# Performance work log

Measured on AMD Instinct MI355X. Metric: run time of the kernel, lower is better.

## Reference

```python
import jax, jax.numpy as jnp
import numpy as np

L, B, D = 50, 1024, 512      # memory slots, batch, d_model
H, DK = 4, 512               # heads, per-head dim (d_k = d_model in this module)
HOP = 3


def setup_inputs() -> dict:
    key = jax.random.key(0)
    ks = jax.random.split(key, 16)
    s = lambda i, shape: jax.random.normal(ks[i], shape, jnp.float32) * 0.02
    return dict(
        momery=jax.random.normal(ks[0], (L, B, D), jnp.float32),
        hid=jax.random.normal(ks[1], (B, D), jnp.float32),
        text_polarity=jax.random.normal(ks[2], (B,), jnp.float32),
        attribute_polarity=jax.random.normal(ks[3], (B,), jnp.float32),
        w=jnp.array(0.5, jnp.float32),
        p_w1=s(4, (D, D)), p_b1=jnp.zeros((D,), jnp.float32),
        p_w2=s(5, (D, D)), p_b2=jnp.zeros((D,), jnp.float32),
        wq=s(6, (D, H * DK)), bq=jnp.zeros((H * DK,), jnp.float32),
        wk=s(7, (D, H * DK)), bk=jnp.zeros((H * DK,), jnp.float32),
        wv=s(8, (D, H * DK)), bv=jnp.zeros((H * DK,), jnp.float32),
        wo=s(9, (H * DK, D)), bo=jnp.zeros((D,), jnp.float32),
    )


def reference(momery, hid, text_polarity, attribute_polarity, w,
              p_w1, p_b1, p_w2, p_b2, wq, bq, wk, bk, wv, bv, wo, bo):
    # k, v depend only on hid (attinkv = hid every hop/slot) -> hoist out of hop loop
    k = (hid @ wk + bk).reshape(B, H, DK)   # [B,H,DK]
    v = (hid @ wv + bv).reshape(B, H, DK)   # [B,H,DK]
    inv_sqrt_dk = jnp.float32(1.0 / np.sqrt(DK))
    for _ in range(HOP):
        # projection MLP over all slots at once (replaces per-slot loop)
        mid = jax.nn.relu(momery @ p_w1 + p_b1) @ p_w2 + p_b2          # [L,B,D]
        q = (mid @ wq + bq).reshape(L, B, H, DK)                        # [L,B,H,DK]
        # single key per query (nk=1): scores [L,B,H,1], softmax -> ones
        scores = (jnp.einsum('lbhd,bhd->lbh', q, k) * inv_sqrt_dk)[..., None]
        att = jax.nn.softmax(scores, axis=-1)                           # [L,B,H,1]
        out = att * v                                                   # [L,B,H,DK]
        temp = out.reshape(L, B, H * DK) @ wo + bo                      # [L,B,D]
        momery = momery + w * temp
    return momery
```

## Files before the change

kernel.cpp:

```cpp
#include <hip/hip_runtime.h>

#define B_SZ 1024
#define D_SZ 512
#define LDSP 68

template <int K, int KCHUNK>
__device__ __forceinline__ void gemm_body(const float* __restrict__ A,
                                          const float* __restrict__ B,
                                          float* __restrict__ C, int N,
                                          int row0, int col0, int zk) {
    __shared__ float As[32 * LDSP];
    __shared__ float Bs[32 * LDSP];

    const int tid = threadIdx.x;
    const int k0  = zk * KCHUNK;
    constexpr int NT = KCHUNK / 32;

    const int aR = tid >> 3;
    const int aK = (tid & 7) << 2;
    const int bK = tid >> 4;
    const int bC = (tid & 15) << 2;

    const int ty = (tid >> 4) << 2;
    const int tx = (tid & 15) << 2;

    const float* pa0 = A + (size_t)(row0 + aR) * K + k0 + aK;
    const float* pa1 = pa0 + (size_t)32 * K;
    const float* pb0 = B + (size_t)(k0 + bK) * N + col0 + bC;
    const float* pb1 = pb0 + (size_t)16 * N;

    float4 a0 = *(const float4*)pa0;
    float4 a1 = *(const float4*)pa1;
    float4 b0 = *(const float4*)pb0;
    float4 b1 = *(const float4*)pb1;

    float acc[4][4] = {};

    for (int t = 0; t < NT; ++t) {
        __syncthreads();
        As[(aK + 0) * LDSP + aR] = a0.x;
        As[(aK + 1) * LDSP + aR] = a0.y;
        As[(aK + 2) * LDSP + aR] = a0.z;
        As[(aK + 3) * LDSP + aR] = a0.w;
        As[(aK + 0) * LDSP + aR + 32] = a1.x;
        As[(aK + 1) * LDSP + aR + 32] = a1.y;
        As[(aK + 2) * LDSP + aR + 32] = a1.z;
        As[(aK + 3) * LDSP + aR + 32] = a1.w;
        *(float4*)(Bs + bK * LDSP + bC) = b0;
        *(float4*)(Bs + (bK + 16) * LDSP + bC) = b1;
        if (t + 1 < NT) {
            pa0 += 32; pa1 += 32;
            pb0 += (size_t)32 * N; pb1 += (size_t)32 * N;
            a0 = *(const float4*)pa0;
            a1 = *(const float4*)pa1;
            b0 = *(const float4*)pb0;
            b1 = *(const float4*)pb1;
        }
        __syncthreads();
#pragma unroll
        for (int kk = 0; kk < 32; ++kk) {
            float4 av = *(const float4*)(As + kk * LDSP + ty);
            float4 bv = *(const float4*)(Bs + kk * LDSP + tx);
            float ar[4] = {av.x, av.y, av.z, av.w};
            float br[4] = {bv.x, bv.y, bv.z, bv.w};
#pragma unroll
            for (int i = 0; i < 4; ++i)
#pragma unroll
                for (int j = 0; j < 4; ++j) acc[i][j] += ar[i] * br[j];
        }
    }

    const int r0 = row0 + ty;
    const int c0 = col0 + tx;
#pragma unroll
    for (int i = 0; i < 4; ++i)
#pragma unroll
        for (int j = 0; j < 4; ++j)
            atomicAdd(&C[(size_t)(r0 + i) * N + c0 + j], acc[i][j]);
}

__global__ __launch_bounds__(256) void gemmA_bias(const float* __restrict__ wv,
                                                  const float* __restrict__ wo,
                                                  const float* __restrict__ bv,
                                                  const float* __restrict__ bo,
                                                  float* __restrict__ W,
                                                  float* __restrict__ b2) {
    if (blockIdx.z == 4) {
        int bid = blockIdx.y * 8 + blockIdx.x;
        int g = bid * 256 + threadIdx.x;
        int o = g & 511;
        int r = g >> 9;
        float s = 0.f;
        int j0 = r * 64;
#pragma unroll 8
        for (int j = j0; j < j0 + 64; ++j) s += bv[j] * wo[j * 512 + o];
        if (r == 0) s += bo[o];
        atomicAdd(&b2[o], s);
        return;
    }
    gemm_body<2048, 512>(wv, wo, W, 512, blockIdx.y * 64, blockIdx.x * 64,
                         blockIdx.z);
}

__global__ __launch_bounds__(256) void gemmB(const float* __restrict__ hid,
                                             const float* __restrict__ W,
                                             float* __restrict__ temp) {
    gemm_body<512, 256>(hid, W, temp, 512, blockIdx.y * 64, blockIdx.x * 64,
                        blockIdx.z);
}

__global__ __launch_bounds__(256) void bcast_add_kernel(const float* __restrict__ mem,
                                                        const float* __restrict__ temp,
                                                        const float* __restrict__ b2,
                                                        const float* __restrict__ wp,
                                                        float* __restrict__ out) {
    int idx = blockIdx.x * 256 + threadIdx.x;
    const float4 mv = ((const float4*)mem)[idx];
    int bd = idx & ((B_SZ * D_SZ / 4) - 1);
    const float4 tv = ((const float4*)temp)[bd];
    const float4 bb = ((const float4*)b2)[bd & 127];
    float s = 3.0f * wp[0];
    float4 o;
    o.x = mv.x + s * (tv.x + bb.x);
    o.y = mv.y + s * (tv.y + bb.y);
    o.z = mv.z + s * (tv.z + bb.z);
    o.w = mv.w + s * (tv.w + bb.w);
    ((float4*)out)[idx] = o;
}

extern "C" void kernel_launch(void* const* d_in, const int* in_sizes, int n_in,
                              void* d_out, int out_size, void* d_ws, size_t ws_size,
                              hipStream_t stream) {
    const float* momery = (const float*)d_in[0];
    const float* hid    = (const float*)d_in[1];
    const float* w      = (const float*)d_in[4];
    const float* wv     = (const float*)d_in[13];
    const float* bv     = (const float*)d_in[14];
    const float* wo     = (const float*)d_in[15];
    const float* bo     = (const float*)d_in[16];
    float* out = (float*)d_out;

    float* W    = (float*)d_ws;
    float* b2   = W + 512 * 512;
    float* temp = b2 + 512;
    size_t zbytes = (size_t)(512 * 512 + 512 + 1024 * 512) * sizeof(float);

    hipMemsetAsync(d_ws, 0, zbytes, stream);

    gemmA_bias<<<dim3(8, 8, 5), 256, 0, stream>>>(wv, wo, bv, bo, W, b2);

    gemmB<<<dim3(8, 16, 2), 256, 0, stream>>>(hid, W, temp);

    bcast_add_kernel<<<25600, 256, 0, stream>>>(momery, temp, b2, w, out);
}
```

Measured before the change: 288.6 us.

## Replace atomic split-K accumulation with partial buffers and drop workspace memset

The split-K GEMMs now write per-split partial results to separate workspace slices with plain float4 stores instead of atomicAdd. The second GEMM sums the four partial W slices as it loads them, and folds the bias partials into its z=0 output. The final broadcast kernel adds the two temp halves. This removes the memset launch and the atomic traffic, at the cost of more workspace and extra reads of the partial buffers.

```diff
diff --git a/kernel.cpp b/kernel.cpp
--- a/kernel.cpp
+++ b/kernel.cpp
@@ -4,29 +4,36 @@
 #define D_SZ 512
 #define LDSP 68
 
-template <int K, int KCHUNK>
-__device__ __forceinline__ void gemm_body(const float* __restrict__ A,
-                                          const float* __restrict__ B,
-                                          float* __restrict__ C, int N,
-                                          int row0, int col0, int zk) {
+__device__ __forceinline__ float4 f4add(float4 a, float4 b) {
+    return make_float4(a.x + b.x, a.y + b.y, a.z + b.z, a.w + b.w);
+}
+
+__global__ __launch_bounds__(256) void gemmA(const float* __restrict__ wv,
+                                             const float* __restrict__ wo,
+                                             const float* __restrict__ bv,
+                                             const float* __restrict__ bo,
+                                             float* __restrict__ Wp,
+                                             float* __restrict__ b2p) {
     __shared__ float As[32 * LDSP];
     __shared__ float Bs[32 * LDSP];
 
-    const int tid = threadIdx.x;
-    const int k0  = zk * KCHUNK;
-    constexpr int NT = KCHUNK / 32;
+    const int tid  = threadIdx.x;
+    const int col0 = blockIdx.x * 64;
+    const int row0 = blockIdx.y * 64;
+    const int z    = blockIdx.z;
+    const int k0   = z * 512;
+    constexpr int K = 2048, N = 512, NT = 16;
 
     const int aR = tid >> 3;
     const int aK = (tid & 7) << 2;
     const int bK = tid >> 4;
     const int bC = (tid & 15) << 2;
-
     const int ty = (tid >> 4) << 2;
     const int tx = (tid & 15) << 2;
 
-    const float* pa0 = A + (size_t)(row0 + aR) * K + k0 + aK;
+    const float* pa0 = wv + (size_t)(row0 + aR) * K + k0 + aK;
     const float* pa1 = pa0 + (size_t)32 * K;
-    const float* pb0 = B + (size_t)(k0 + bK) * N + col0 + bC;
+    const float* pb0 = wo + (size_t)(k0 + bK) * N + col0 + bC;
     const float* pb1 = pb0 + (size_t)16 * N;
 
     float4 a0 = *(const float4*)pa0;
@@ -60,9 +67,9 @@
 #pragma unroll
         for (int kk = 0; kk < 32; ++kk) {
             float4 av = *(const float4*)(As + kk * LDSP + ty);
-            float4 bv = *(const float4*)(Bs + kk * LDSP + tx);
+            float4 bv4 = *(const float4*)(Bs + kk * LDSP + tx);
             float ar[4] = {av.x, av.y, av.z, av.w};
-            float br[4] = {bv.x, bv.y, bv.z, bv.w};
+            float br[4] = {bv4.x, bv4.y, bv4.z, bv4.w};
 #pragma unroll
             for (int i = 0; i < 4; ++i)
 #pragma unroll
@@ -70,61 +77,139 @@
         }
     }
 
-    const int r0 = row0 + ty;
-    const int c0 = col0 + tx;
+    float* C = Wp + (size_t)z * 262144;
+    const int r0 = row0 + ty, c0 = col0 + tx;
 #pragma unroll
     for (int i = 0; i < 4; ++i)
-#pragma unroll
-        for (int j = 0; j < 4; ++j)
-            atomicAdd(&C[(size_t)(r0 + i) * N + c0 + j], acc[i][j]);
-}
-
-__global__ __launch_bounds__(256) void gemmA_bias(const float* __restrict__ wv,
-                                                  const float* __restrict__ wo,
-                                                  const float* __restrict__ bv,
-                                                  const float* __restrict__ bo,
-                                                  float* __restrict__ W,
-                                                  float* __restrict__ b2) {
-    if (blockIdx.z == 4) {
+        *(float4*)(C + (size_t)(r0 + i) * N + c0) =
+            make_float4(acc[i][0], acc[i][1], acc[i][2], acc[i][3]);
+
+    if (z == 0) {
         int bid = blockIdx.y * 8 + blockIdx.x;
-        int g = bid * 256 + threadIdx.x;
+        int g = bid * 256 + tid;
         int o = g & 511;
         int r = g >> 9;
-        float s = 0.f;
+        float s = (r == 0) ? bo[o] : 0.f;
         int j0 = r * 64;
 #pragma unroll 8
         for (int j = j0; j < j0 + 64; ++j) s += bv[j] * wo[j * 512 + o];
-        if (r == 0) s += bo[o];
-        atomicAdd(&b2[o], s);
-        return;
-    }
-    gemm_body<2048, 512>(wv, wo, W, 512, blockIdx.y * 64, blockIdx.x * 64,
-                         blockIdx.z);
+        b2p[r * 512 + o] = s;
+    }
 }
 
 __global__ __launch_bounds__(256) void gemmB(const float* __restrict__ hid,
-                                             const float* __restrict__ W,
-                                             float* __restrict__ temp) {
-    gemm_body<512, 256>(hid, W, temp, 512, blockIdx.y * 64, blockIdx.x * 64,
-                        blockIdx.z);
+                                             const float* __restrict__ Wp,
+                                             const float* __restrict__ b2p,
+                                             float* __restrict__ t0,
+                                             float* __restrict__ t1) {
+    __shared__ float As[32 * LDSP];
+    __shared__ float Bs[32 * LDSP];
+
+    const int tid  = threadIdx.x;
+    const int col0 = blockIdx.x * 64;
+    const int row0 = blockIdx.y * 64;
+    const int z    = blockIdx.z;
+    const int k0   = z * 256;
+    constexpr int K = 512, N = 512, NT = 8;
+
+    const int aR = tid >> 3;
+    const int aK = (tid & 7) << 2;
+    const int bK = tid >> 4;
+    const int bC = (tid & 15) << 2;
+    const int ty = (tid >> 4) << 2;
+    const int tx = (tid & 15) << 2;
+
+    const float* pa0 = hid + (size_t)(row0 + aR) * K + k0 + aK;
+    const float* pa1 = pa0 + (size_t)32 * K;
+    const float* pb0 = Wp + (size_t)(k0 + bK) * N + col0 + bC;
+    const float* pb1 = pb0 + (size_t)16 * N;
+
+    float4 a0 = *(const float4*)pa0;
+    float4 a1 = *(const float4*)pa1;
+    float4 vb0[4], vb1[4];
+#pragma unroll
+    for (int p = 0; p < 4; ++p) {
+        vb0[p] = *(const float4*)(pb0 + (size_t)p * 262144);
+        vb1[p] = *(const float4*)(pb1 + (size_t)p * 262144);
+    }
+
+    float acc[4][4] = {};
+
+    for (int t = 0; t < NT; ++t) {
+        float4 sb0 = f4add(f4add(vb0[0], vb0[1]), f4add(vb0[2], vb0[3]));
+        float4 sb1 = f4add(f4add(vb1[0], vb1[1]), f4add(vb1[2], vb1[3]));
+        __syncthreads();
+        As[(aK + 0) * LDSP + aR] = a0.x;
+        As[(aK + 1) * LDSP + aR] = a0.y;
+        As[(aK + 2) * LDSP + aR] = a0.z;
+        As[(aK + 3) * LDSP + aR] = a0.w;
+        As[(aK + 0) * LDSP + aR + 32] = a1.x;
+        As[(aK + 1) * LDSP + aR + 32] = a1.y;
+        As[(aK + 2) * LDSP + aR + 32] = a1.z;
+        As[(aK + 3) * LDSP + aR + 32] = a1.w;
+        *(float4*)(Bs + bK * LDSP + bC) = sb0;
+        *(float4*)(Bs + (bK + 16) * LDSP + bC) = sb1;
+        if (t + 1 < NT) {
+            pa0 += 32; pa1 += 32;
+            pb0 += (size_t)32 * N; pb1 += (size_t)32 * N;
+            a0 = *(const float4*)pa0;
+            a1 = *(const float4*)pa1;
+#pragma unroll
+            for (int p = 0; p < 4; ++p) {
+                vb0[p] = *(const float4*)(pb0 + (size_t)p * 262144);
+                vb1[p] = *(const float4*)(pb1 + (size_t)p * 262144);
+            }
+        }
+        __syncthreads();
+#pragma unroll
+        for (int kk = 0; kk < 32; ++kk) {
+            float4 av = *(const float4*)(As + kk * LDSP + ty);
+            float4 bv4 = *(const float4*)(Bs + kk * LDSP + tx);
+            float ar[4] = {av.x, av.y, av.z, av.w};
+            float br[4] = {bv4.x, bv4.y, bv4.z, bv4.w};
+#pragma unroll
+            for (int i = 0; i < 4; ++i)
+#pragma unroll
+                for (int j = 0; j < 4; ++j) acc[i][j] += ar[i] * br[j];
+        }
+    }
+
+    __syncthreads();
+    if (z == 0 && tid < 64) {
+        float s = 0.f;
+#pragma unroll 8
+        for (int r = 0; r < 32; ++r) s += b2p[r * 512 + col0 + tid];
+        Bs[tid] = s;
+    }
+    __syncthreads();
+    float4 bb = make_float4(0, 0, 0, 0);
+    if (z == 0) bb = *(const float4*)(Bs + tx);
+
+    float* C = z ? t1 : t0;
+    const int r0 = row0 + ty, c0 = col0 + tx;
+#pragma unroll
+    for (int i = 0; i < 4; ++i)
+        *(float4*)(C + (size_t)(r0 + i) * N + c0) =
+            make_float4(acc[i][0] + bb.x, acc[i][1] + bb.y,
+                        acc[i][2] + bb.z, acc[i][3] + bb.w);
 }
 
 __global__ __launch_bounds__(256) void bcast_add_kernel(const float* __restrict__ mem,
-                                                        const float* __restrict__ temp,
-                                                        const float* __restrict__ b2,
+                                                        const float* __restrict__ t0,
+                                                        const float* __restrict__ t1,
                                                         const float* __restrict__ wp,
                                                         float* __restrict__ out) {
     int idx = blockIdx.x * 256 + threadIdx.x;
     const float4 mv = ((const float4*)mem)[idx];
     int bd = idx & ((B_SZ * D_SZ / 4) - 1);
-    const float4 tv = ((const float4*)temp)[bd];
-    const float4 bb = ((const float4*)b2)[bd & 127];
+    const float4 a = ((const float4*)t0)[bd];
+    const float4 b = ((const float4*)t1)[bd];
     float s = 3.0f * wp[0];
     float4 o;
-    o.x = mv.x + s * (tv.x + bb.x);
-    o.y = mv.y + s * (tv.y + bb.y);
-    o.z = mv.z + s * (tv.z + bb.z);
-    o.w = mv.w + s * (tv.w + bb.w);
+    o.x = mv.x + s * (a.x + b.x);
+    o.y = mv.y + s * (a.y + b.y);
+    o.z = mv.z + s * (a.z + b.z);
+    o.w = mv.w + s * (a.w + b.w);
     ((float4*)out)[idx] = o;
 }
 
@@ -140,16 +225,14 @@
     const float* bo     = (const float*)d_in[16];
     float* out = (float*)d_out;
 
-    float* W    = (float*)d_ws;
-    float* b2   = W + 512 * 512;
-    float* temp = b2 + 512;
-    size_t zbytes = (size_t)(512 * 512 + 512 + 1024 * 512) * sizeof(float);
-
-    hipMemsetAsync(d_ws, 0, zbytes, stream);
-
-    gemmA_bias<<<dim3(8, 8, 5), 256, 0, stream>>>(wv, wo, bv, bo, W, b2);
-
-    gemmB<<<dim3(8, 16, 2), 256, 0, stream>>>(hid, W, temp);
-
-    bcast_add_kernel<<<25600, 256, 0, stream>>>(momery, temp, b2, w, out);
-}
+    float* Wp  = (float*)d_ws;
+    float* b2p = Wp + 4 * 262144;
+    float* t0  = b2p + 16384;
+    float* t1  = t0 + 524288;
+
+    gemmA<<<dim3(8, 8, 4), 256, 0, stream>>>(wv, wo, bv, bo, Wp, b2p);
+
+    gemmB<<<dim3(8, 16, 2), 256, 0, stream>>>(hid, Wp, b2p, t0, t1);
+
+    bcast_add_kernel<<<25600, 256, 0, stream>>>(momery, t0, t1, w, out);
+}
```

Result: faster. 257.4 us (-10.8%).
